# Optimization experiments

Hardware: AMD Instinct MI355X
Metric: run time of the kernel (lower is better)

Reference implementation:

```python
import jax, jax.numpy as jnp
import numpy as np
import math

ANCHORS = np.array([[12., 16.], [19., 36.], [40., 28.]], dtype=np.float32)
NUM_CLASSES = 80
IMG_DIM = 608.0
NUM_ANCHORS = 3


def setup_inputs() -> dict:
    key = jax.random.key(0)
    ks = jax.random.split(key, 9)
    B, A, G, NC = 16, NUM_ANCHORS, 76, NUM_CLASSES
    x = jax.random.normal(ks[0], (B, A * (NC + 5), G, G), jnp.float32)
    iou = jax.random.uniform(ks[1], (B, A, G, G), jnp.float32, 0.0, 0.95)
    obj_mask = jax.random.bernoulli(ks[2], 0.02, (B, A, G, G))
    noobj_mask = jnp.logical_and(~obj_mask, jax.random.bernoulli(ks[3], 0.95, (B, A, G, G)))
    tw = jax.random.uniform(ks[4], (B, A, G, G), jnp.float32, 0.1, 4.0)
    th = jax.random.uniform(ks[5], (B, A, G, G), jnp.float32, 0.1, 4.0)
    tcls = jax.random.uniform(ks[6], (B, A, G, G, NC), jnp.float32)
    tconf = jax.random.uniform(ks[7], (B, A, G, G), jnp.float32)
    tb = jax.random.uniform(ks[8], (B, A, G, G, 4), jnp.float32)
    # target boxes in grid units: centers in [0,G), sizes in (0.5, 8.5)
    target_boxes = jnp.concatenate([tb[..., :2] * G, tb[..., 2:] * 8.0 + 0.5], -1)
    return {"x": x, "iou": iou, "obj_mask": obj_mask, "noobj_mask": noobj_mask,
            "tw": tw, "th": th, "tcls": tcls, "tconf": tconf, "target_boxes": target_boxes}


def _clog(p):
    # torch F.binary_cross_entropy clamps log to -100
    return jnp.maximum(jnp.log(p), -100.0)


def _bce(p, t):
    return -(t * _clog(p) + (1.0 - t) * _clog(1.0 - p))


def yolo_forward(x, iou, obj_mask, noobj_mask, tw, th, tcls, tconf, target_boxes):
    B = x.shape[0]
    G = x.shape[2]
    A, NC = NUM_ANCHORS, NUM_CLASSES
    stride = IMG_DIM / G
    # [B, A, G, G, 5+NC]
    pred = x.reshape(B, A, NC + 5, G, G).transpose(0, 1, 3, 4, 2)
    px = jax.nn.sigmoid(pred[..., 0])
    py = jax.nn.sigmoid(pred[..., 1])
    pw = pred[..., 2]
    ph = pred[..., 3]
    pconf = jax.nn.sigmoid(pred[..., 4])
    pcls = jax.nn.sigmoid(pred[..., 5:])

    scaled = jnp.asarray(ANCHORS) / stride
    gx = jnp.arange(G, dtype=x.dtype)[None, None, None, :]
    gy = jnp.arange(G, dtype=x.dtype)[None, None, :, None]
    aw = scaled[:, 0][None, :, None, None]
    ah = scaled[:, 1][None, :, None, None]

    bx = px + gx
    by = py + gy
    bw = jnp.exp(pw) * aw
    bh = jnp.exp(ph) * ah
    pred_boxes = jnp.stack([bx, by, bw, bh], -1)

    output = jnp.concatenate([
        pred_boxes.reshape(B, -1, 4) * stride,
        pconf.reshape(B, -1, 1),
        pcls.reshape(B, -1, NC)], -1)

    # ---- loss (masked CIoU + BCE), computed dense then mask-reduced ----
    m = obj_mask.astype(x.dtype)
    nm = noobj_mask.astype(x.dtype)
    txc, tyc, twd, tht = (target_boxes[..., i] for i in range(4))

    tx1, ty1 = txc - twd / 2, tyc - tht / 2
    tx2, ty2 = txc + twd / 2, tyc + tht / 2
    px1, py1 = bx - bw / 2, by - bh / 2
    px2, py2 = bx + bw / 2, by + bh / 2

    xc1 = jnp.minimum(px1, tx1)
    yc1 = jnp.minimum(py1, ty1)
    xc2 = jnp.maximum(px2, tx2)
    yc2 = jnp.maximum(py2, ty2)

    c = (xc2 - xc1) ** 2 + (yc2 - yc1) ** 2 + 1e-07
    d = (txc - bx) ** 2 + (tyc - by) ** 2
    rDIoU = d / c
    v = (4.0 / math.pi ** 2) * (jnp.arctan(tw / th) - jnp.arctan(pw / ph)) ** 2
    S = 1.0 - iou
    alpha = jax.lax.stop_gradient(v / (S + v))  # torch.no_grad() block
    ciou_term = 1.0 - iou + rDIoU + alpha * v
    CIoUloss = jnp.sum(m * ciou_term) / B

    cnt_obj = jnp.maximum(jnp.sum(m), 1.0)
    cnt_noobj = jnp.maximum(jnp.sum(nm), 1.0)
    bce_conf = _bce(pconf, tconf)
    loss_conf = 1.0 * jnp.sum(m * bce_conf) / cnt_obj + 100.0 * jnp.sum(nm * bce_conf) / cnt_noobj
    loss_cls = jnp.sum(m[..., None] * _bce(pcls, tcls)) / (cnt_obj * NUM_CLASSES)

    total_loss = CIoUloss + loss_conf + loss_cls
    return output, total_loss


def reference(x, iou, obj_mask, noobj_mask, tw, th, tcls, tconf, target_boxes):
    return yolo_forward(x, iou, obj_mask, noobj_mask, tw, th, tcls, tconf, target_boxes)
```

## Files before the change

### kernel.cpp

```cpp
#include <hip/hip_runtime.h>

#define B_ 16
#define A_ 3
#define G_ 76
#define GG_ (G_*G_)
#define NC_ 80
#define C_ 85
#define NCELL (B_*A_*GG_)
#define OUTN ((size_t)NCELL*C_)
#define NBLKM (NCELL/64)
#define NSLOT (C_*16)

typedef float f4 __attribute__((ext_vector_type(4)));

__device__ __forceinline__ float sigf(float v){ return 1.0f/(1.0f + __expf(-v)); }
__device__ __forceinline__ float clog_(float p){ return fmaxf(__logf(p), -100.0f); }
__device__ __forceinline__ float bcef(float p, float t){ return -(t*clog_(p) + (1.0f-t)*clog_(1.0f-p)); }

__global__ __launch_bounds__(256, 6) void mega_kernel(
        const float* __restrict__ x, const float* __restrict__ iou,
        const unsigned int* __restrict__ om, const unsigned int* __restrict__ nm,
        const float* __restrict__ tw, const float* __restrict__ th,
        const float* __restrict__ tcls, const float* __restrict__ tconf,
        const float* __restrict__ tbox,
        float* __restrict__ out, float* __restrict__ partials){
    __shared__ __align__(16) float lds[64*C_];
    __shared__ float praw[64][2];
    __shared__ float sred[4][6];

    const int tid  = (int)threadIdx.x;
    const int w    = tid >> 6;
    const int lane = tid & 63;

    unsigned qd8 = NBLKM >> 3, rr = NBLKM & 7u;
    unsigned xcd = blockIdx.x & 7u, seq = blockIdx.x >> 3;
    int blk = (int)((xcd < rr ? xcd*(qd8+1u) : rr*(qd8+1u) + (xcd-rr)*qd8) + seq);
    int n0 = blk*64;

    f4 rv[6];
    #pragma unroll
    for (int it=0; it<6; ++it){
        int idx = tid + it*256;
        if (idx < NSLOT){
            int k = idx >> 4, q = idx & 15;
            int cell0 = n0 + 4*q;
            int ba = cell0 / GG_;
            int ij0 = cell0 - ba*GG_;
            rv[it] = *(const f4*)(x + ((size_t)ba*C_ + (size_t)k)*GG_ + ij0);
        }
    }

    #pragma unroll
    for (int it=0; it<6; ++it){
        int idx = tid + it*256;
        if (idx < NSLOT){
            int k = idx >> 4, q = idx & 15;
            int cell0 = n0 + 4*q;
            int ba = cell0 / GG_;
            int ij0 = cell0 - ba*GG_;
            int in_ = ij0 / G_;
            int jn0 = ij0 - in_*G_;
            int a = ba % A_;
            int lc0 = 4*q;
            f4 v = rv[it];
            f4 r;
            if (k >= 4){
                r[0]=sigf(v[0]); r[1]=sigf(v[1]); r[2]=sigf(v[2]); r[3]=sigf(v[3]);
            } else if (k == 0){
                float j0 = (float)jn0;
                r[0]=(sigf(v[0])+j0)*8.0f;      r[1]=(sigf(v[1])+j0+1.0f)*8.0f;
                r[2]=(sigf(v[2])+j0+2.0f)*8.0f; r[3]=(sigf(v[3])+j0+3.0f)*8.0f;
            } else if (k == 1){
                float fi = (float)in_;
                r[0]=(sigf(v[0])+fi)*8.0f; r[1]=(sigf(v[1])+fi)*8.0f;
                r[2]=(sigf(v[2])+fi)*8.0f; r[3]=(sigf(v[3])+fi)*8.0f;
            } else if (k == 2){
                float aw8 = (a==0)?12.0f:((a==1)?19.0f:40.0f);
                r[0]=__expf(v[0])*aw8; r[1]=__expf(v[1])*aw8;
                r[2]=__expf(v[2])*aw8; r[3]=__expf(v[3])*aw8;
                praw[lc0+0][0]=v[0]; praw[lc0+1][0]=v[1];
                praw[lc0+2][0]=v[2]; praw[lc0+3][0]=v[3];
            } else {
                float ah8 = (a==0)?16.0f:((a==1)?36.0f:28.0f);
                r[0]=__expf(v[0])*ah8; r[1]=__expf(v[1])*ah8;
                r[2]=__expf(v[2])*ah8; r[3]=__expf(v[3])*ah8;
                praw[lc0+0][1]=v[0]; praw[lc0+1][1]=v[1];
                praw[lc0+2][1]=v[2]; praw[lc0+3][1]=v[3];
            }
            int bix = lc0*C_ + k;
            lds[bix]       = r[0];
            lds[bix+C_]    = r[1];
            lds[bix+2*C_]  = r[2];
            lds[bix+3*C_]  = r[3];
        }
    }
    __syncthreads();

    {
        const f4* src4 = (const f4*)lds;
        f4* dst4 = (f4*)(out + (size_t)n0*C_);
        #pragma unroll
        for (int it=0; it<6; ++it){
            int f = tid + it*256;
            if (f < NSLOT) dst4[f] = src4[f];
        }
    }

    int lc = tid >> 2, qd = tid & 3;
    int n  = n0 + lc;
    bool obj   = om[n] != 0u;
    bool noobj = nm[n] != 0u;
    const float* lrow = lds + lc*C_;

    float cls = 0.f;
    if (obj){
        const float* tcl = tcls + (size_t)n*NC_ + qd*20;
        const float* lp  = lrow + 5 + qd*20;
        #pragma unroll 4
        for (int j=0; j<20; ++j) cls += bcef(lp[j], tcl[j]);
    }
    cls += __shfl_xor(cls, 1, 64);
    cls += __shfl_xor(cls, 2, 64);
    if (qd != 0) cls = 0.f;

    float ciou=0.f, co=0.f, cn=0.f;
    if (qd == 0 && obj){
        float bx = lrow[0]*0.125f, by = lrow[1]*0.125f;
        float bw = lrow[2]*0.125f, bh = lrow[3]*0.125f;
        float rwv = praw[lc][0], rhv = praw[lc][1];
        float iouv = iou[n], twv = tw[n], thv = th[n];
        f4 tb = *(const f4*)(tbox + (size_t)n*4);
        float txc=tb[0], tyc=tb[1], twd=tb[2], tht=tb[3];
        float tx1 = txc - twd*0.5f, ty1 = tyc - tht*0.5f;
        float tx2 = txc + twd*0.5f, ty2 = tyc + tht*0.5f;
        float px1 = bx - bw*0.5f,  py1 = by - bh*0.5f;
        float px2 = bx + bw*0.5f,  py2 = by + bh*0.5f;
        float xc1 = fminf(px1, tx1), yc1 = fminf(py1, ty1);
        float xc2 = fmaxf(px2, tx2), yc2 = fmaxf(py2, ty2);
        float cc = (xc2-xc1)*(xc2-xc1) + (yc2-yc1)*(yc2-yc1) + 1e-7f;
        float dd = (txc-bx)*(txc-bx) + (tyc-by)*(tyc-by);
        float rdiou = dd/cc;
        float dat = atanf(twv/thv) - atanf(rwv/rhv);
        float vv = 0.40528473456935108577f * dat*dat;
        float Si = 1.0f - iouv;
        float alpha = vv/(Si+vv);
        ciou = 1.0f - iouv + rdiou + alpha*vv;
    }
    if (qd == 1 && (obj || noobj)){
        float bc = bcef(lrow[4], tconf[n]);
        co = obj ? bc : 0.f;
        cn = noobj ? bc : 0.f;
    }
    unsigned long long bo  = __ballot(obj   && qd == 0);
    unsigned long long bn2 = __ballot(noobj && qd == 1);

    float vals[4] = {ciou, co, cn, cls};
    #pragma unroll
    for (int q2=0; q2<4; ++q2){
        float v = vals[q2];
        #pragma unroll
        for (int o=32; o>0; o>>=1) v += __shfl_xor(v, o, 64);
        vals[q2] = v;
    }
    if (lane == 0){
        sred[w][0]=vals[0]; sred[w][1]=vals[1]; sred[w][2]=vals[2]; sred[w][3]=vals[3];
        sred[w][4]=(float)__popcll(bo); sred[w][5]=(float)__popcll(bn2);
    }
    __syncthreads();
    if (tid < 6)
        partials[(size_t)tid*NBLKM + blk] = sred[0][tid]+sred[1][tid]+sred[2][tid]+sred[3][tid];
}

__global__ __launch_bounds__(256) void final_kernel(const float* __restrict__ partials,
                                                    float* __restrict__ out_loss){
    double acc[6] = {0,0,0,0,0,0};
    for (int idx = (int)threadIdx.x; idx < NBLKM; idx += 256){
        #pragma unroll
        for (int q=0;q<6;q++) acc[q] += (double)partials[(size_t)q*NBLKM + idx];
    }
    #pragma unroll
    for (int q=0;q<6;q++){
        double v = acc[q];
        #pragma unroll
        for (int o=32;o>0;o>>=1) v += __shfl_xor(v, o, 64);
        acc[q] = v;
    }
    __shared__ double smd[6][4];
    int lane = (int)threadIdx.x & 63, wid = (int)threadIdx.x >> 6;
    if (lane == 0){
        #pragma unroll
        for (int q=0;q<6;q++) smd[q][wid] = acc[q];
    }
    __syncthreads();
    if (threadIdx.x == 0){
        double s[6];
        #pragma unroll
        for (int q=0;q<6;q++) s[q] = smd[q][0]+smd[q][1]+smd[q][2]+smd[q][3];
        double cnt_o = fmax(s[4], 1.0);
        double cnt_n = fmax(s[5], 1.0);
        double total = s[0]/(double)B_
                     + s[1]/cnt_o
                     + 100.0*s[2]/cnt_n
                     + s[3]/(cnt_o*(double)NC_);
        *out_loss = (float)total;
    }
}

extern "C" void kernel_launch(void* const* d_in, const int* in_sizes, int n_in,
                              void* d_out, int out_size, void* d_ws, size_t ws_size,
                              hipStream_t stream){
    const float* x     = (const float*)d_in[0];
    const float* iou   = (const float*)d_in[1];
    const unsigned int* om = (const unsigned int*)d_in[2];
    const unsigned int* nm = (const unsigned int*)d_in[3];
    const float* tw    = (const float*)d_in[4];
    const float* th    = (const float*)d_in[5];
    const float* tcls  = (const float*)d_in[6];
    const float* tconf = (const float*)d_in[7];
    const float* tbox  = (const float*)d_in[8];
    float* out = (float*)d_out;

    float* partials = (float*)d_ws;

    mega_kernel<<<NBLKM, 256, 0, stream>>>(x, iou, om, nm, tw, th, tcls, tconf, tbox,
                                           out, partials);
    final_kernel<<<1, 256, 0, stream>>>(partials, out + OUTN);
}
```

Baseline: 49.08 us.

## Make waves independent per 16-cell tile and fuse final reduction via last-block atomic

Each wave now loads, transforms, stages and stores its own 16-cell slice in a private LDS region, which removes the block-wide barrier between the transform and the output copy. Output stores become nontemporal. The separate final reduction kernel is replaced by a last-block-done pattern using an atomic counter that is zeroed with a memset before launch. Launch bounds drop from 6 to 4 blocks per CU. The memset adds a small launch, and the last block performs a serial tail reduction.

```diff
diff --git a/kernel.cpp b/kernel.cpp
--- a/kernel.cpp
+++ b/kernel.cpp
@@ -9,7 +9,7 @@
 #define NCELL (B_*A_*GG_)
 #define OUTN ((size_t)NCELL*C_)
 #define NBLKM (NCELL/64)
-#define NSLOT (C_*16)
+#define WSLOT 340
 
 typedef float f4 __attribute__((ext_vector_type(4)));
 
@@ -17,16 +17,18 @@
 __device__ __forceinline__ float clog_(float p){ return fmaxf(__logf(p), -100.0f); }
 __device__ __forceinline__ float bcef(float p, float t){ return -(t*clog_(p) + (1.0f-t)*clog_(1.0f-p)); }
 
-__global__ __launch_bounds__(256, 6) void mega_kernel(
+__global__ __launch_bounds__(256, 4) void mega_kernel(
         const float* __restrict__ x, const float* __restrict__ iou,
         const unsigned int* __restrict__ om, const unsigned int* __restrict__ nm,
         const float* __restrict__ tw, const float* __restrict__ th,
         const float* __restrict__ tcls, const float* __restrict__ tconf,
         const float* __restrict__ tbox,
-        float* __restrict__ out, float* __restrict__ partials){
-    __shared__ __align__(16) float lds[64*C_];
+        float* __restrict__ out, float* __restrict__ partials,
+        unsigned int* __restrict__ cnt, float* __restrict__ out_loss){
+    __shared__ __align__(16) float lds[4][16*C_];
     __shared__ float praw[64][2];
     __shared__ float sred[4][6];
+    __shared__ unsigned int lastflag;
 
     const int tid  = (int)threadIdx.x;
     const int w    = tid >> 6;
@@ -35,82 +37,80 @@
     unsigned qd8 = NBLKM >> 3, rr = NBLKM & 7u;
     unsigned xcd = blockIdx.x & 7u, seq = blockIdx.x >> 3;
     int blk = (int)((xcd < rr ? xcd*(qd8+1u) : rr*(qd8+1u) + (xcd-rr)*qd8) + seq);
-    int n0 = blk*64;
+
+    int nw  = blk*64 + w*16;
+    int ba  = nw / GG_;
+    int ijw = nw - ba*GG_;
+    int a   = ba % A_;
+    float aw8 = (a==0)?12.0f:((a==1)?19.0f:40.0f);
+    float ah8 = (a==0)?16.0f:((a==1)?36.0f:28.0f);
+    const float* xw = x + (size_t)ba*C_*GG_ + (size_t)ijw;
+    float* ldsw = lds[w];
 
     f4 rv[6];
     #pragma unroll
     for (int it=0; it<6; ++it){
-        int idx = tid + it*256;
-        if (idx < NSLOT){
-            int k = idx >> 4, q = idx & 15;
-            int cell0 = n0 + 4*q;
-            int ba = cell0 / GG_;
-            int ij0 = cell0 - ba*GG_;
-            rv[it] = *(const f4*)(x + ((size_t)ba*C_ + (size_t)k)*GG_ + ij0);
+        int s = lane + it*64;
+        if (s < WSLOT){
+            int k = s >> 2, q = s & 3;
+            rv[it] = *(const f4*)(xw + (size_t)k*GG_ + 4*q);
         }
     }
 
     #pragma unroll
     for (int it=0; it<6; ++it){
-        int idx = tid + it*256;
-        if (idx < NSLOT){
-            int k = idx >> 4, q = idx & 15;
-            int cell0 = n0 + 4*q;
-            int ba = cell0 / GG_;
-            int ij0 = cell0 - ba*GG_;
-            int in_ = ij0 / G_;
-            int jn0 = ij0 - in_*G_;
-            int a = ba % A_;
-            int lc0 = 4*q;
+        int s = lane + it*64;
+        if (s < WSLOT){
+            int k = s >> 2, q = s & 3;
+            int ij0 = ijw + 4*q;
             f4 v = rv[it];
             f4 r;
             if (k >= 4){
                 r[0]=sigf(v[0]); r[1]=sigf(v[1]); r[2]=sigf(v[2]); r[3]=sigf(v[3]);
             } else if (k == 0){
-                float j0 = (float)jn0;
+                float j0 = (float)(ij0 - (ij0/G_)*G_);
                 r[0]=(sigf(v[0])+j0)*8.0f;      r[1]=(sigf(v[1])+j0+1.0f)*8.0f;
                 r[2]=(sigf(v[2])+j0+2.0f)*8.0f; r[3]=(sigf(v[3])+j0+3.0f)*8.0f;
             } else if (k == 1){
-                float fi = (float)in_;
+                float fi = (float)(ij0/G_);
                 r[0]=(sigf(v[0])+fi)*8.0f; r[1]=(sigf(v[1])+fi)*8.0f;
                 r[2]=(sigf(v[2])+fi)*8.0f; r[3]=(sigf(v[3])+fi)*8.0f;
             } else if (k == 2){
-                float aw8 = (a==0)?12.0f:((a==1)?19.0f:40.0f);
                 r[0]=__expf(v[0])*aw8; r[1]=__expf(v[1])*aw8;
                 r[2]=__expf(v[2])*aw8; r[3]=__expf(v[3])*aw8;
-                praw[lc0+0][0]=v[0]; praw[lc0+1][0]=v[1];
-                praw[lc0+2][0]=v[2]; praw[lc0+3][0]=v[3];
+                int c0 = w*16 + 4*q;
+                praw[c0+0][0]=v[0]; praw[c0+1][0]=v[1];
+                praw[c0+2][0]=v[2]; praw[c0+3][0]=v[3];
             } else {
-                float ah8 = (a==0)?16.0f:((a==1)?36.0f:28.0f);
                 r[0]=__expf(v[0])*ah8; r[1]=__expf(v[1])*ah8;
                 r[2]=__expf(v[2])*ah8; r[3]=__expf(v[3])*ah8;
-                praw[lc0+0][1]=v[0]; praw[lc0+1][1]=v[1];
-                praw[lc0+2][1]=v[2]; praw[lc0+3][1]=v[3];
+                int c0 = w*16 + 4*q;
+                praw[c0+0][1]=v[0]; praw[c0+1][1]=v[1];
+                praw[c0+2][1]=v[2]; praw[c0+3][1]=v[3];
             }
-            int bix = lc0*C_ + k;
-            lds[bix]       = r[0];
-            lds[bix+C_]    = r[1];
-            lds[bix+2*C_]  = r[2];
-            lds[bix+3*C_]  = r[3];
-        }
-    }
-    __syncthreads();
+            int bix = 4*q*C_ + k;
+            ldsw[bix]      = r[0];
+            ldsw[bix+C_]   = r[1];
+            ldsw[bix+2*C_] = r[2];
+            ldsw[bix+3*C_] = r[3];
+        }
+    }
 
     {
-        const f4* src4 = (const f4*)lds;
-        f4* dst4 = (f4*)(out + (size_t)n0*C_);
+        const f4* src4 = (const f4*)ldsw;
+        f4* dst4 = (f4*)(out + (size_t)nw*C_);
         #pragma unroll
         for (int it=0; it<6; ++it){
-            int f = tid + it*256;
-            if (f < NSLOT) dst4[f] = src4[f];
-        }
-    }
-
-    int lc = tid >> 2, qd = tid & 3;
-    int n  = n0 + lc;
+            int s = lane + it*64;
+            if (s < WSLOT) __builtin_nontemporal_store(src4[s], dst4 + s);
+        }
+    }
+
+    int lc = lane >> 2, qd = lane & 3;
+    int n  = nw + lc;
     bool obj   = om[n] != 0u;
     bool noobj = nm[n] != 0u;
-    const float* lrow = lds + lc*C_;
+    const float* lrow = ldsw + lc*C_;
 
     float cls = 0.f;
     if (obj){
@@ -127,7 +127,7 @@
     if (qd == 0 && obj){
         float bx = lrow[0]*0.125f, by = lrow[1]*0.125f;
         float bw = lrow[2]*0.125f, bh = lrow[3]*0.125f;
-        float rwv = praw[lc][0], rhv = praw[lc][1];
+        float rwv = praw[w*16+lc][0], rhv = praw[w*16+lc][1];
         float iouv = iou[n], twv = tw[n], thv = th[n];
         f4 tb = *(const f4*)(tbox + (size_t)n*4);
         float txc=tb[0], tyc=tb[1], twd=tb[2], tht=tb[3];
@@ -169,40 +169,45 @@
     __syncthreads();
     if (tid < 6)
         partials[(size_t)tid*NBLKM + blk] = sred[0][tid]+sred[1][tid]+sred[2][tid]+sred[3][tid];
-}
-
-__global__ __launch_bounds__(256) void final_kernel(const float* __restrict__ partials,
-                                                    float* __restrict__ out_loss){
-    double acc[6] = {0,0,0,0,0,0};
-    for (int idx = (int)threadIdx.x; idx < NBLKM; idx += 256){
+
+    if (tid == 0){
+        __threadfence();
+        unsigned int prev = atomicAdd(cnt, 1u);
+        lastflag = (prev == (unsigned)(NBLKM-1)) ? 1u : 0u;
+    }
+    __syncthreads();
+    if (lastflag){
+        __threadfence();
+        double acc[6] = {0,0,0,0,0,0};
+        for (int idx = tid; idx < NBLKM; idx += 256){
+            #pragma unroll
+            for (int q=0;q<6;q++) acc[q] += (double)partials[(size_t)q*NBLKM + idx];
+        }
         #pragma unroll
-        for (int q=0;q<6;q++) acc[q] += (double)partials[(size_t)q*NBLKM + idx];
-    }
-    #pragma unroll
-    for (int q=0;q<6;q++){
-        double v = acc[q];
-        #pragma unroll
-        for (int o=32;o>0;o>>=1) v += __shfl_xor(v, o, 64);
-        acc[q] = v;
-    }
-    __shared__ double smd[6][4];
-    int lane = (int)threadIdx.x & 63, wid = (int)threadIdx.x >> 6;
-    if (lane == 0){
-        #pragma unroll
-        for (int q=0;q<6;q++) smd[q][wid] = acc[q];
-    }
-    __syncthreads();
-    if (threadIdx.x == 0){
-        double s[6];
-        #pragma unroll
-        for (int q=0;q<6;q++) s[q] = smd[q][0]+smd[q][1]+smd[q][2]+smd[q][3];
-        double cnt_o = fmax(s[4], 1.0);
-        double cnt_n = fmax(s[5], 1.0);
-        double total = s[0]/(double)B_
-                     + s[1]/cnt_o
-                     + 100.0*s[2]/cnt_n
-                     + s[3]/(cnt_o*(double)NC_);
-        *out_loss = (float)total;
+        for (int q=0;q<6;q++){
+            double v = acc[q];
+            #pragma unroll
+            for (int o=32;o>0;o>>=1) v += __shfl_xor(v, o, 64);
+            acc[q] = v;
+        }
+        __shared__ double smd[6][4];
+        if (lane == 0){
+            #pragma unroll
+            for (int q=0;q<6;q++) smd[q][w] = acc[q];
+        }
+        __syncthreads();
+        if (tid == 0){
+            double s[6];
+            #pragma unroll
+            for (int q=0;q<6;q++) s[q] = smd[q][0]+smd[q][1]+smd[q][2]+smd[q][3];
+            double cnt_o = fmax(s[4], 1.0);
+            double cnt_n = fmax(s[5], 1.0);
+            double total = s[0]/(double)B_
+                         + s[1]/cnt_o
+                         + 100.0*s[2]/cnt_n
+                         + s[3]/(cnt_o*(double)NC_);
+            *out_loss = (float)total;
+        }
     }
 }
 
@@ -220,9 +225,10 @@
     const float* tbox  = (const float*)d_in[8];
     float* out = (float*)d_out;
 
-    float* partials = (float*)d_ws;
-
+    unsigned int* cnt = (unsigned int*)d_ws;
+    float* partials = (float*)((char*)d_ws + 64);
+
+    hipMemsetAsync(d_ws, 0, 64, stream);
     mega_kernel<<<NBLKM, 256, 0, stream>>>(x, iou, om, nm, tw, th, tcls, tconf, tbox,
-                                           out, partials);
-    final_kernel<<<1, 256, 0, stream>>>(partials, out + OUTN);
+                                           out, partials, cnt, out + OUTN);
 }
```

After: 193.7 us. 295% more time.
